# Kernel optimization log

Hardware: AMD Instinct MI355X
Metric: run time of the kernel (lower is better)

## Reference

```python
import jax, jax.numpy as jnp
import numpy as np

B, L, H = 32, 1024, 1024  # kv_length must equal hidden_size for the bmm to typecheck


def setup_inputs() -> dict:
    key = jax.random.key(0)
    ks = jax.random.split(key, 9)
    s = 0.02  # small init so tanh does not saturate
    return {
        "query": jax.random.normal(ks[0], (B, L, H), dtype=jnp.float32),
        "key": jax.random.normal(ks[1], (B, L, H), dtype=jnp.float32),
        "value": jax.random.normal(ks[2], (B, L, H), dtype=jnp.float32),
        "w1_w": jax.random.normal(ks[3], (H, H), dtype=jnp.float32) * s,
        "w1_b": jax.random.normal(ks[4], (H,), dtype=jnp.float32) * s,
        "w2_w": jax.random.normal(ks[5], (H, H), dtype=jnp.float32) * s,
        "w2_b": jax.random.normal(ks[6], (H,), dtype=jnp.float32) * s,
        "v_w": jax.random.normal(ks[7], (H, H), dtype=jnp.float32) * s,
        "v_b": jax.random.normal(ks[8], (H,), dtype=jnp.float32) * s,
    }


def reference(query, key, value, w1_w, w1_b, w2_w, w2_b, v_w, v_b):
    # score_fn: v(tanh(w1(query) + w2(value))); `key` is unused (del key in source)
    h = jnp.tanh(jnp.einsum("blh,oh->blo", query, w1_w) + w1_b
                 + jnp.einsum("blh,oh->blo", value, w2_w) + w2_b)  # (B, L, H)
    score = jnp.einsum("blh,oh->blo", h, v_w) + v_b                 # (B, L, H)
    attention_weights = jax.nn.softmax(score, axis=-1)              # (B, L, H)
    # torch.bmm(weights, value): contracts weights' last dim (H) with value's kv dim (==H)
    context_vector = jnp.einsum("blk,bkh->blh", attention_weights, value)
    return (attention_weights, context_vector)
```

## Files before the change

kernel.cpp:

```cpp
#include <hip/hip_runtime.h>
#include <cstdint>

using u16 = unsigned short;
using u32 = unsigned int;
typedef __attribute__((ext_vector_type(4))) float f32x4;
typedef __attribute__((ext_vector_type(8))) short short8;
typedef __attribute__((ext_vector_type(4))) u16 u16x4;
typedef __attribute__((ext_vector_type(8))) u16 u16x8;

__device__ __forceinline__ u16 f2bf(float f) {
  u32 u = __builtin_bit_cast(u32, f);
  u += 0x7FFFu + ((u >> 16) & 1u);
  return (u16)(u >> 16);
}
__device__ __forceinline__ float bf2f(u16 x) {
  return __builtin_bit_cast(float, (u32)x << 16);
}

__device__ __forceinline__ void gload16(const void* g, void* l) {
  __builtin_amdgcn_global_load_lds(
      (const __attribute__((address_space(1))) void*)g,
      (__attribute__((address_space(3))) void*)l, 16, 0, 0);
}

__device__ __forceinline__ float fast_tanh(float x) {
  float ax = fabsf(x);
  float e = __expf(-2.0f * ax);
  float r = (1.0f - e) / (1.0f + e);
  return x < 0.0f ? -r : r;
}

#define SBAR() do { asm volatile("" ::: "memory"); __builtin_amdgcn_s_barrier(); asm volatile("" ::: "memory"); } while (0)

template<int N> __device__ __forceinline__ void vmw() {
  if constexpr (N == 10) asm volatile("s_waitcnt vmcnt(10)" ::: "memory");
  else if constexpr (N == 8) asm volatile("s_waitcnt vmcnt(8)" ::: "memory");
  else if constexpr (N == 6) asm volatile("s_waitcnt vmcnt(6)" ::: "memory");
  else if constexpr (N == 4) asm volatile("s_waitcnt vmcnt(4)" ::: "memory");
  else if constexpr (N == 2) asm volatile("s_waitcnt vmcnt(2)" ::: "memory");
  else if constexpr (N == 0) asm volatile("s_waitcnt vmcnt(0)" ::: "memory");
}

__device__ __forceinline__ int swz(int L) { return L ^ (((L >> 9) & 1) << 5); }

__device__ __forceinline__ void swz_mn256(int bid, int& m0, int& n0) {
  int s = (bid & 7) * 64 + (bid >> 3);
  n0 = (s & 3) << 8;
  m0 = (s >> 2) << 8;
}

__global__ void cvt_ker(const float4* __restrict__ src, u16x4* __restrict__ dst, int n4) {
  int i = blockIdx.x * 256 + threadIdx.x;
  if (i < n4) {
    float4 f = src[i];
    u16x4 o = { f2bf(f.x), f2bf(f.y), f2bf(f.z), f2bf(f.w) };
    dst[i] = o;
  }
}

__device__ __forceinline__ void stage_half(
    const u16* __restrict__ A0, const u16* __restrict__ B0,
    const u16* __restrict__ A1, const u16* __restrict__ B1,
    int half_nt, u16* lds, int j, int m0, int n0, int w, int rc0, int rc1)
{
  int jt = j >> 2, hh = j & 3;
  int kk = hh >> 1, isA = hh & 1;
  const u16* src;
  int kt;
  if (jt < half_nt) { src = isA ? A0 : B0; kt = jt; }
  else              { src = isA ? A1 : B1; kt = jt - half_nt; }
  int base_row = isA ? m0 : n0;
  int koff = kt * 64 + kk * 32;
  u16* dst = lds + ((jt & 1) * 4 + hh) * 8192 + w * 512;
  const u16* g0 = src + (size_t)base_row * 1024 + koff;
  gload16(g0 + rc0, dst);
  gload16(g0 + rc1, dst + 4096);
}

__device__ __forceinline__ void rdB4(short8* d, const u16* lds, int buf, int kk, const int* boff) {
  const char* h = (const char*)(lds + (buf * 4 + kk * 2) * 8192);
  d[0] = *(const short8*)(h + boff[0]);
  d[1] = *(const short8*)(h + boff[1]);
  d[2] = *(const short8*)(h + boff[2]);
  d[3] = *(const short8*)(h + boff[3]);
}
__device__ __forceinline__ void rdA4(short8* d, const u16* lds, int buf, int kk, int mh, const int* aoff) {
  const char* h = (const char*)(lds + (buf * 4 + 1 + kk * 2) * 8192);
  d[0] = *(const short8*)(h + aoff[mh * 4 + 0]);
  d[1] = *(const short8*)(h + aoff[mh * 4 + 1]);
  d[2] = *(const short8*)(h + aoff[mh * 4 + 2]);
  d[3] = *(const short8*)(h + aoff[mh * 4 + 3]);
}

#define MFMA16(AS, BS, BASE) do {                                                   \
  __builtin_amdgcn_s_setprio(1);                                                    \
  _Pragma("unroll")                                                                 \
  for (int ni_ = 0; ni_ < 4; ni_++) {                                               \
    acc[(BASE)+0][ni_] = __builtin_amdgcn_mfma_f32_16x16x32_bf16(AS[0], BS[ni_], acc[(BASE)+0][ni_], 0, 0, 0); \
    acc[(BASE)+1][ni_] = __builtin_amdgcn_mfma_f32_16x16x32_bf16(AS[1], BS[ni_], acc[(BASE)+1][ni_], 0, 0, 0); \
    acc[(BASE)+2][ni_] = __builtin_amdgcn_mfma_f32_16x16x32_bf16(AS[2], BS[ni_], acc[(BASE)+2][ni_], 0, 0, 0); \
    acc[(BASE)+3][ni_] = __builtin_amdgcn_mfma_f32_16x16x32_bf16(AS[3], BS[ni_], acc[(BASE)+3][ni_], 0, 0, 0); \
  }                                                                                 \
  __builtin_amdgcn_s_setprio(0);                                                    \
} while (0)

#define TILE(T, V0, V1, V2, V3, S0_, S1_, S2_, S3_, NX) do {                        \
  const int buf_ = (T) & 1;                                                         \
                            \
  rdA4(a1s, lds, buf_, 0, 1, aoff);                                                 \
  if (S0_) stage_half(A0, B0, A1, B1, half_nt, lds, 4 * (T) + 7, m0, n0, w, rc0, rc1); \
  MFMA16(a0s, b0s, 0);                                                              \
  vmw<V0>(); SBAR();                                                                \
               \
  rdB4(b1s, lds, buf_, 1, boff);                                                    \
  rdA4(a0s, lds, buf_, 1, 0, aoff);                                                 \
  if (S1_) stage_half(A0, B0, A1, B1, half_nt, lds, 4 * (T) + 8, m0, n0, w, rc0, rc1); \
  MFMA16(a1s, b0s, 4);                                                              \
  vmw<V1>(); SBAR();                                                                \
                            \
  rdA4(a1s, lds, buf_, 1, 1, aoff);                                                 \
  if (S2_) stage_half(A0, B0, A1, B1, half_nt, lds, 4 * (T) + 9, m0, n0, w, rc0, rc1); \
  MFMA16(a0s, b1s, 0);                                                              \
  vmw<V2>(); SBAR();                                                                \
   \
  if (NX) { rdB4(b0s, lds, buf_ ^ 1, 0, boff); rdA4(a0s, lds, buf_ ^ 1, 0, 0, aoff); } \
  if (S3_) stage_half(A0, B0, A1, B1, half_nt, lds, 4 * (T) + 10, m0, n0, w, rc0, rc1); \
  MFMA16(a1s, b1s, 4);                                                              \
  vmw<V3>(); SBAR();                                                                \
} while (0)

__device__ __forceinline__ void gemm_loop(
    const u16* __restrict__ A0, const u16* __restrict__ B0,
    const u16* __restrict__ A1, const u16* __restrict__ B1,
    int half_nt, int NT, int m0, int n0, u16* lds, f32x4 acc[8][4])
{
  const int tid = threadIdx.x;
  const int w = tid >> 6, lane = tid & 63;
  const int wr = w >> 2, wc = w & 3;
  const int lr = lane & 15, g = lane >> 4;

  int rc0, rc1;
  {
    int seg0 = w * 64 + lane, seg1 = 512 + w * 64 + lane;
    int L0 = swz(seg0 * 16), L1 = swz(seg1 * 16);
    rc0 = (L0 >> 6) * 1024 + ((L0 & 63) >> 1);
    rc1 = (L1 >> 6) * 1024 + ((L1 & 63) >> 1);
  }
  int aoff[8], boff[4];
  #pragma unroll
  for (int mi = 0; mi < 8; mi++)
    aoff[mi] = swz((wr * 128 + mi * 16 + lr) * 64 + g * 16);
  #pragma unroll
  for (int ni = 0; ni < 4; ni++)
    boff[ni] = swz((wc * 64 + ni * 16 + lr) * 64 + g * 16);

  short8 a0s[4], a1s[4], b0s[4], b1s[4];

  #pragma unroll
  for (int j = 0; j < 7; j++)
    stage_half(A0, B0, A1, B1, half_nt, lds, j, m0, n0, w, rc0, rc1);
  vmw<10>();
  SBAR();
  rdB4(b0s, lds, 0, 0, boff);
  rdA4(a0s, lds, 0, 0, 0, aoff);

  for (int t = 0; t < NT - 2; t += 2) {
    TILE(t,     8, 8, 8, 8, 1, 1, 1, 1, true);
    TILE(t + 1, 8, 8, 8, 8, 1, 1, 1, 1, true);
  }
  TILE(NT - 2, 8, 8, 4, 4, 1, 0, 0, 0, true);
  TILE(NT - 1, 0, 0, -1, -1, 0, 0, 0, 0, false);
}

__global__ void __launch_bounds__(512, 2)
gemm1_ker(const u16* __restrict__ q, const u16* __restrict__ v,
          const u16* __restrict__ w1, const u16* __restrict__ w2,
          const float* __restrict__ b1, const float* __restrict__ b2,
          u16* __restrict__ H)
{
  __shared__ u16 lds[65536];
  int m0, n0;
  swz_mn256(blockIdx.x, m0, n0);
  f32x4 acc[8][4];
  #pragma unroll
  for (int mi = 0; mi < 8; mi++)
    #pragma unroll
    for (int ni = 0; ni < 4; ni++) acc[mi][ni] = (f32x4){0.f, 0.f, 0.f, 0.f};

  gemm_loop(q, w1, v, w2, 16, 32, m0, n0, lds, acc);

  int tid = threadIdx.x, w = tid >> 6, lane = tid & 63;
  int wr = w >> 2, wc = w & 3, lr = lane & 15, g = lane >> 4;
  #pragma unroll
  for (int ni = 0; ni < 4; ni++) {
    int col = n0 + wc * 64 + ni * 16 + lr;
    float bias = b1[col] + b2[col];
    #pragma unroll
    for (int mi = 0; mi < 8; mi++)
      #pragma unroll
      for (int r = 0; r < 4; r++) {
        int row = m0 + wr * 128 + mi * 16 + g * 4 + r;
        H[(size_t)row * 1024 + col] = f2bf(fast_tanh(acc[mi][ni][r] + bias));
      }
  }
}

__global__ void __launch_bounds__(512, 2)
escore_ker(const u16* __restrict__ h, const u16* __restrict__ vw,
           const float* __restrict__ vb, u16* __restrict__ E,
           float* __restrict__ partial)
{
  __shared__ u16 lds[65536];
  int m0, n0;
  swz_mn256(blockIdx.x, m0, n0);
  f32x4 acc[8][4];
  #pragma unroll
  for (int mi = 0; mi < 8; mi++)
    #pragma unroll
    for (int ni = 0; ni < 4; ni++) acc[mi][ni] = (f32x4){0.f, 0.f, 0.f, 0.f};

  gemm_loop(h, vw, h, vw, 16, 16, m0, n0, lds, acc);

  int tid = threadIdx.x, w = tid >> 6, lane = tid & 63;
  int wr = w >> 2, wc = w & 3, lr = lane & 15, g = lane >> 4;

  #pragma unroll
  for (int ni = 0; ni < 4; ni++) {
    float vbc = vb[n0 + wc * 64 + ni * 16 + lr];
    #pragma unroll
    for (int mi = 0; mi < 8; mi++)
      #pragma unroll
      for (int r = 0; r < 4; r++)
        acc[mi][ni][r] = __expf(acc[mi][ni][r] + vbc);
  }

  __syncthreads();
  float* ps = (float*)lds;
  #pragma unroll
  for (int mi = 0; mi < 8; mi++) {
    #pragma unroll
    for (int r = 0; r < 4; r++) {
      float t = acc[mi][0][r] + acc[mi][1][r] + acc[mi][2][r] + acc[mi][3][r];
      t += __shfl_xor(t, 1, 64);
      t += __shfl_xor(t, 2, 64);
      t += __shfl_xor(t, 4, 64);
      t += __shfl_xor(t, 8, 64);
      if (lr == 0) ps[wc * 256 + wr * 128 + mi * 16 + g * 4 + r] = t;
    }
  }
  __syncthreads();
  if (tid < 256) {
    float s = ps[tid] + ps[256 + tid] + ps[512 + tid] + ps[768 + tid];
    partial[(size_t)(n0 >> 8) * 32768 + m0 + tid] = s;
  }

  #pragma unroll
  for (int ni = 0; ni < 4; ni++) {
    int col = n0 + wc * 64 + ni * 16 + lr;
    #pragma unroll
    for (int mi = 0; mi < 8; mi++)
      #pragma unroll
      for (int r = 0; r < 4; r++) {
        int row = m0 + wr * 128 + mi * 16 + g * 4 + r;
        E[(size_t)row * 1024 + col] = f2bf(acc[mi][ni][r]);
      }
  }
}

__global__ void rowsum_ker(const float* __restrict__ partial, float* __restrict__ inv) {
  int r = blockIdx.x * 256 + threadIdx.x;
  float s = partial[r] + partial[32768 + r] + partial[65536 + r] + partial[98304 + r];
  inv[r] = 1.0f / s;
}

__global__ void wout_ker(const u16* __restrict__ E, const float* __restrict__ inv,
                         float* __restrict__ out) {
  int t = blockIdx.x * 256 + threadIdx.x;
  size_t base = (size_t)t * 8;
  float sc = inv[t >> 7];
  u16x8 v = *(const u16x8*)(E + base);
  float4 o0, o1;
  o0.x = bf2f(v[0]) * sc; o0.y = bf2f(v[1]) * sc; o0.z = bf2f(v[2]) * sc; o0.w = bf2f(v[3]) * sc;
  o1.x = bf2f(v[4]) * sc; o1.y = bf2f(v[5]) * sc; o1.z = bf2f(v[6]) * sc; o1.w = bf2f(v[7]) * sc;
  *(float4*)(out + base) = o0;
  *(float4*)(out + base + 4) = o1;
}

__global__ void transpose_ker(const u16* __restrict__ in, u16* __restrict__ out) {
  __shared__ u16 tile[64][68];
  int b = blockIdx.z;
  int h0 = blockIdx.x * 64, l0 = blockIdx.y * 64;
  const u16* src = in + (size_t)b * 1048576;
  u16* dst = out + (size_t)b * 1048576;
  int t = threadIdx.x;
  #pragma unroll
  for (int i = 0; i < 4; i++) {
    int idx = i * 1024 + t * 4;
    int r = idx >> 6, c = idx & 63;
    *(u16x4*)&tile[r][c] = *(const u16x4*)&src[(size_t)(l0 + r) * 1024 + h0 + c];
  }
  __syncthreads();
  #pragma unroll
  for (int i = 0; i < 4; i++) {
    int idx = i * 1024 + t * 4;
    int hr = idx >> 6, lc = idx & 63;
    u16x4 val = { tile[lc][hr], tile[lc + 1][hr], tile[lc + 2][hr], tile[lc + 3][hr] };
    *(u16x4*)&dst[(size_t)(h0 + hr) * 1024 + l0 + lc] = val;
  }
}

__global__ void __launch_bounds__(512, 2)
gemm3_ker(const u16* __restrict__ E, const u16* __restrict__ vT,
          const float* __restrict__ inv, float* __restrict__ ctx)
{
  __shared__ u16 lds[65536];
  int m0, n0;
  swz_mn256(blockIdx.x, m0, n0);
  const u16* Bb = vT + (size_t)(m0 >> 10) * 1048576;
  f32x4 acc[8][4];
  #pragma unroll
  for (int mi = 0; mi < 8; mi++)
    #pragma unroll
    for (int ni = 0; ni < 4; ni++) acc[mi][ni] = (f32x4){0.f, 0.f, 0.f, 0.f};

  gemm_loop(E, Bb, E, Bb, 16, 16, m0, n0, lds, acc);

  int tid = threadIdx.x, w = tid >> 6, lane = tid & 63;
  int wr = w >> 2, wc = w & 3, lr = lane & 15, g = lane >> 4;
  #pragma unroll
  for (int mi = 0; mi < 8; mi++) {
    #pragma unroll
    for (int r = 0; r < 4; r++) {
      int row = m0 + wr * 128 + mi * 16 + g * 4 + r;
      float sc = inv[row];
      #pragma unroll
      for (int ni = 0; ni < 4; ni++) {
        int col = n0 + wc * 64 + ni * 16 + lr;
        ctx[(size_t)row * 1024 + col] = acc[mi][ni][r] * sc;
      }
    }
  }
}

extern "C" void kernel_launch(void* const* d_in, const int* in_sizes, int n_in,
                              void* d_out, int out_size, void* d_ws, size_t ws_size,
                              hipStream_t stream) {
  const float* q   = (const float*)d_in[0];
  const float* v   = (const float*)d_in[2];
  const float* w1w = (const float*)d_in[3];
  const float* b1  = (const float*)d_in[4];
  const float* w2w = (const float*)d_in[5];
  const float* b2  = (const float*)d_in[6];
  const float* vww = (const float*)d_in[7];
  const float* vb  = (const float*)d_in[8];

  float* out_w = (float*)d_out;
  float* out_c = out_w + (size_t)33554432;

  u16* q_bf  = (u16*)d_ws;
  u16* v_bf  = q_bf + 33554432;
  u16* h_bf  = v_bf + 33554432;
  u16* w1_bf = h_bf + 33554432;
  u16* w2_bf = w1_bf + 1048576;
  u16* vw_bf = w2_bf + 1048576;
  u16* wsm_bf = q_bf;
  u16* vT_bf  = h_bf;
  float* partial = (float*)w1_bf;
  float* invp    = (float*)w2_bf;

  if (ws_size < (size_t)207618048) return;

  cvt_ker<<<32768, 256, 0, stream>>>((const float4*)q,   (u16x4*)q_bf,  8388608);
  cvt_ker<<<32768, 256, 0, stream>>>((const float4*)v,   (u16x4*)v_bf,  8388608);
  cvt_ker<<<1024,  256, 0, stream>>>((const float4*)w1w, (u16x4*)w1_bf, 262144);
  cvt_ker<<<1024,  256, 0, stream>>>((const float4*)w2w, (u16x4*)w2_bf, 262144);
  cvt_ker<<<1024,  256, 0, stream>>>((const float4*)vww, (u16x4*)vw_bf, 262144);

  gemm1_ker<<<512, 512, 0, stream>>>(q_bf, v_bf, w1_bf, w2_bf, b1, b2, h_bf);
  escore_ker<<<512, 512, 0, stream>>>(h_bf, vw_bf, vb, wsm_bf, partial);
  rowsum_ker<<<128, 256, 0, stream>>>(partial, invp);
  transpose_ker<<<dim3(16, 16, 32), 256, 0, stream>>>(v_bf, vT_bf);
  wout_ker<<<16384, 256, 0, stream>>>(wsm_bf, invp, out_w);
  gemm3_ker<<<512, 512, 0, stream>>>(wsm_bf, vT_bf, invp, out_c);
}
```

Baseline: 455.9 us.

## Fuse attention-weight output into gemm3 epilogue and retune gemm main-loop wait counts

The separate wout kernel, which read the bf16 unnormalized scores and wrote normalized fp32 attention weights, is removed. Its work moves into the gemm3 epilogue: each block writes the 256x256 tile of normalized weights it owns, reading E that was likely just streamed through cache. The gemm main loop is also rewritten from a 2x-unrolled loop into a peeled first tile plus a single-step loop with different wait/barrier parameters. This saves one launch and possibly an extra read of E, at the cost of a longer gemm3 epilogue and some risk in the changed pipeline wait counts.

```diff
diff --git a/kernel.cpp b/kernel.cpp
--- a/kernel.cpp
+++ b/kernel.cpp
@@ -164,12 +164,11 @@
   rdB4(b0s, lds, 0, 0, boff);
   rdA4(a0s, lds, 0, 0, 0, aoff);
 
-  for (int t = 0; t < NT - 2; t += 2) {
-    TILE(t,     8, 8, 8, 8, 1, 1, 1, 1, true);
-    TILE(t + 1, 8, 8, 8, 8, 1, 1, 1, 1, true);
-  }
-  TILE(NT - 2, 8, 8, 4, 4, 1, 0, 0, 0, true);
-  TILE(NT - 1, 0, 0, -1, -1, 0, 0, 0, 0, false);
+  TILE(0, 8, -1, 8, 4, 1, 1, 1, 1, true);
+  for (int t = 1; t < NT - 2; ++t)
+    TILE(t, -1, -1, -1, 4, 1, 1, 1, 1, true);
+  TILE(NT - 2, -1, -1, -1, 0, 1, 0, 0, 0, true);
+  TILE(NT - 1, -1, -1, -1, -1, 0, 0, 0, 0, false);
 }
 
 __global__ void __launch_bounds__(512, 2)
@@ -273,19 +272,6 @@
   inv[r] = 1.0f / s;
 }
 
-__global__ void wout_ker(const u16* __restrict__ E, const float* __restrict__ inv,
-                         float* __restrict__ out) {
-  int t = blockIdx.x * 256 + threadIdx.x;
-  size_t base = (size_t)t * 8;
-  float sc = inv[t >> 7];
-  u16x8 v = *(const u16x8*)(E + base);
-  float4 o0, o1;
-  o0.x = bf2f(v[0]) * sc; o0.y = bf2f(v[1]) * sc; o0.z = bf2f(v[2]) * sc; o0.w = bf2f(v[3]) * sc;
-  o1.x = bf2f(v[4]) * sc; o1.y = bf2f(v[5]) * sc; o1.z = bf2f(v[6]) * sc; o1.w = bf2f(v[7]) * sc;
-  *(float4*)(out + base) = o0;
-  *(float4*)(out + base + 4) = o1;
-}
-
 __global__ void transpose_ker(const u16* __restrict__ in, u16* __restrict__ out) {
   __shared__ u16 tile[64][68];
   int b = blockIdx.z;
@@ -311,7 +297,8 @@
 
 __global__ void __launch_bounds__(512, 2)
 gemm3_ker(const u16* __restrict__ E, const u16* __restrict__ vT,
-          const float* __restrict__ inv, float* __restrict__ ctx)
+          const float* __restrict__ inv, float* __restrict__ ctx,
+          float* __restrict__ out_w)
 {
   __shared__ u16 lds[65536];
   int m0, n0;
@@ -339,6 +326,26 @@
         ctx[(size_t)row * 1024 + col] = acc[mi][ni][r] * sc;
       }
     }
+  }
+
+  #pragma unroll
+  for (int i = 0; i < 8; i++) {
+    int row = i * 32 + (tid >> 4);
+    int col = (tid & 15) * 16;
+    const u16* es = E + (size_t)(m0 + row) * 1024 + n0 + col;
+    float* wd = out_w + (size_t)(m0 + row) * 1024 + n0 + col;
+    float sc = inv[m0 + row];
+    u16x8 v0 = *(const u16x8*)es;
+    u16x8 v1 = *(const u16x8*)(es + 8);
+    float4 o;
+    o.x = bf2f(v0[0]) * sc; o.y = bf2f(v0[1]) * sc; o.z = bf2f(v0[2]) * sc; o.w = bf2f(v0[3]) * sc;
+    *(float4*)wd = o;
+    o.x = bf2f(v0[4]) * sc; o.y = bf2f(v0[5]) * sc; o.z = bf2f(v0[6]) * sc; o.w = bf2f(v0[7]) * sc;
+    *(float4*)(wd + 4) = o;
+    o.x = bf2f(v1[0]) * sc; o.y = bf2f(v1[1]) * sc; o.z = bf2f(v1[2]) * sc; o.w = bf2f(v1[3]) * sc;
+    *(float4*)(wd + 8) = o;
+    o.x = bf2f(v1[4]) * sc; o.y = bf2f(v1[5]) * sc; o.z = bf2f(v1[6]) * sc; o.w = bf2f(v1[7]) * sc;
+    *(float4*)(wd + 12) = o;
   }
 }
 
@@ -380,6 +387,5 @@
   escore_ker<<<512, 512, 0, stream>>>(h_bf, vw_bf, vb, wsm_bf, partial);
   rowsum_ker<<<128, 256, 0, stream>>>(partial, invp);
   transpose_ker<<<dim3(16, 16, 32), 256, 0, stream>>>(v_bf, vT_bf);
-  wout_ker<<<16384, 256, 0, stream>>>(wsm_bf, invp, out_w);
-  gemm3_ker<<<512, 512, 0, stream>>>(wsm_bf, vT_bf, invp, out_c);
-}
+  gemm3_ker<<<512, 512, 0, stream>>>(wsm_bf, vT_bf, invp, out_c, out_w);
+}
```

After: 463.4 us. No clear change (+1.7%).
